# Kernel optimization log

Hardware: AMD Instinct MI355X
Metric: run time of the kernel (lower is better)

Reference implementation:

```python
import jax, jax.numpy as jnp
import numpy as np

IN_DIM = 256
HIDDEN = 512
MEM = 256
IN_LEN = 4096
THETA = 4096.0
BATCH = 32


def _expm(M):
    # scaling-and-squaring with Taylor series (float64)
    nrm = max(np.linalg.norm(M, 1), 1e-30)
    s = max(0, int(np.ceil(np.log2(nrm))) + 1)
    A = M / (2.0 ** s)
    d = M.shape[0]
    E = np.eye(d)
    term = np.eye(d)
    for k in range(1, 30):
        term = term @ A / k
        E = E + term
    for _ in range(s):
        E = E @ E
    return E


def _gen_AB(memory_size, theta):
    Q = np.arange(memory_size, dtype=np.float64).reshape(-1, 1)
    R = (2 * Q + 1) / theta
    i, j = np.meshgrid(Q, Q, indexing='ij')
    A = np.where(i < j, -1.0, (-1.0) ** (i - j + 1)) * R
    B = (-1.0) ** Q * R  # [mem, 1]
    # ZOH discretization with dt=1: expm of augmented [[A,B],[0,0]]
    d = memory_size
    em = np.zeros((d + 1, d + 1))
    em[:d, :d] = A
    em[:d, d:] = B
    ed = _expm(em)
    Ad = ed[:d, :d]
    Bd = ed[:d, d:]
    return Ad, Bd


def _impulse(memory_size, in_len, theta):
    Ad, Bd = _gen_AB(memory_size, theta)
    H = np.empty((memory_size, in_len), dtype=np.float64)
    v = Bd.copy()  # [mem, 1]
    for t in range(in_len):
        H[:, t] = v[:, 0]
        v = Ad @ v
    return H.astype(np.float32)


def setup_inputs() -> dict:
    key = jax.random.key(0)
    kx, ku, kh = jax.random.split(key, 3)
    x = jax.random.normal(kx, (BATCH, IN_LEN, IN_DIM), dtype=jnp.float32)
    W_u = jax.random.normal(ku, (1, IN_DIM), dtype=jnp.float32)
    W_h = jax.random.normal(kh, (HIDDEN, MEM + IN_DIM), dtype=jnp.float32)
    H = jnp.asarray(_impulse(MEM, IN_LEN, THETA))  # [mem, in_len]
    return {"x": x, "W_u": W_u, "W_h": W_h, "H": H}


def reference(x, W_u, W_h, H):
    batch, n, _ = x.shape
    # encode: u = relu(x @ W_u^T)  -> [B, n, 1]
    u = jax.nn.relu(jnp.einsum('bni,oi->bno', x, W_u))
    # FFT long convolution with impulse response H
    u_fft = jnp.fft.rfft(u.transpose(0, 2, 1), n=2 * n, axis=-1)  # [B,1,n+1]
    H_fft = jnp.fft.rfft(H, n=2 * n, axis=-1)                      # [mem,n+1]
    m = jnp.fft.irfft(u_fft * H_fft[None], n=2 * n, axis=-1)       # [B,mem,2n]
    m = m[:, :, :n].transpose(0, 2, 1)                             # [B,n,mem]
    # output head: h = relu([m, x] @ W_h^T)
    input_h = jnp.concatenate((m, x), axis=-1)                     # [B,n,mem+in_dim]
    h = jax.nn.relu(jnp.einsum('bnc,oc->bno', input_h, W_h))       # [B,n,hidden]
    h_n = h[:, -1, :]
    return (h, h_n)
```

## Files before the change

### kernel.cpp

```cpp
#include <hip/hip_runtime.h>
#include <hip/hip_bf16.h>
#include <math.h>


#define BATCH 32
#define T     4096
#define IND   256
#define HID   512
#define MEM   256
#define FFT_N 8192
#define FFT_LOG 13
#define BT    131072

typedef __attribute__((ext_vector_type(8))) short short8;
typedef __attribute__((ext_vector_type(8))) _Float16 half8;
typedef __attribute__((ext_vector_type(4))) float f32x4;

__device__ inline short f2bf(float f) {
    unsigned u = __float_as_uint(f);
    unsigned r = (u + 0x7FFFu + ((u >> 16) & 1u)) >> 16;
    return (short)r;
}
__device__ inline unsigned pk2h(float a, float b) {
    union { _Float16 h[2]; unsigned u; } v;
    v.h[0] = (_Float16)a; v.h[1] = (_Float16)b;
    return v.u;
}

__global__ __launch_bounds__(256) void relu_u_kernel(const float* __restrict__ x,
                                                     const float* __restrict__ Wu,
                                                     float* __restrict__ u,
                                                     _Float16* __restrict__ xh) {
    int wave = threadIdx.x >> 6, lane = threadIdx.x & 63;
    int r = blockIdx.x * 4 + wave;
    const float4 xv = *(const float4*)(x + (size_t)r * IND + lane * 4);
    const float4 wv = *(const float4*)(Wu + lane * 4);
    union { _Float16 h[4]; uint2 u2; } hv;
    hv.h[0] = (_Float16)xv.x; hv.h[1] = (_Float16)xv.y;
    hv.h[2] = (_Float16)xv.z; hv.h[3] = (_Float16)xv.w;
    *(uint2*)(xh + (size_t)r * IND + lane * 4) = hv.u2;
    float acc = xv.x * wv.x + xv.y * wv.y + xv.z * wv.z + xv.w * wv.w;
    for (int off = 32; off; off >>= 1) acc += __shfl_down(acc, off);
    if (lane == 0) u[r] = fmaxf(acc, 0.f);
}

__global__ __launch_bounds__(256) void wh_half_kernel(const float* __restrict__ Wh,
                                                      _Float16* __restrict__ whf) {
    int i = blockIdx.x * 256 + threadIdx.x;
    float4 v = *(const float4*)(Wh + (size_t)i * 4);
    union { _Float16 h[4]; uint2 u2; } hv;
    hv.h[0] = (_Float16)v.x; hv.h[1] = (_Float16)v.y;
    hv.h[2] = (_Float16)v.z; hv.h[3] = (_Float16)v.w;
    *(uint2*)(whf + (size_t)i * 4) = hv.u2;
}

__device__ void fft_fwd_r4(float* re, float* im) {
    __syncthreads();
    {
        const float fm = -(float)M_PI / 4096.f;
#pragma unroll
        for (int s = 0; s < 8; ++s) {
            int k = threadIdx.x + s * 512;
            float sn, cs; __sincosf(fm * (float)k, &sn, &cs);
            float ar = re[k], ai = im[k], br = re[k + 4096], bi = im[k + 4096];
            re[k] = ar + br; im[k] = ai + bi;
            float dr = ar - br, di = ai - bi;
            re[k + 4096] = cs * dr - sn * di;
            im[k + 4096] = cs * di + sn * dr;
        }
        __syncthreads();
    }
    for (int st = 10; st >= 0; st -= 2) {
        int q = 1 << st;
        float fm = -(float)M_PI / (float)(2 * q);
#pragma unroll
        for (int s = 0; s < 4; ++s) {
            int k = threadIdx.x + s * 512;
            int j = k & (q - 1);
            int i0 = ((k >> st) << (st + 2)) + j;
            float ar = re[i0],         ai = im[i0];
            float br = re[i0 + q],     bi = im[i0 + q];
            float cr = re[i0 + 2 * q], ci = im[i0 + 2 * q];
            float dr = re[i0 + 3 * q], di = im[i0 + 3 * q];
            float t0r = ar + cr, t0i = ai + ci;
            float t1r = ar - cr, t1i = ai - ci;
            float t2r = br + dr, t2i = bi + di;
            float t3r = bi - di, t3i = dr - br;
            float sn, cs; __sincosf(fm * (float)j, &sn, &cs);
            float w2r = cs * cs - sn * sn, w2i = 2.f * cs * sn;
            float w3r = w2r * cs - w2i * sn, w3i = w2r * sn + w2i * cs;
            re[i0] = t0r + t2r;               im[i0] = t0i + t2i;
            float er = t0r - t2r, ei = t0i - t2i;
            re[i0 + q] = er * w2r - ei * w2i; im[i0 + q] = er * w2i + ei * w2r;
            float fr = t1r + t3r, fi = t1i + t3i;
            re[i0 + 2 * q] = fr * cs - fi * sn; im[i0 + 2 * q] = fr * sn + fi * cs;
            float gr = t1r - t3r, gi = t1i - t3i;
            re[i0 + 3 * q] = gr * w3r - gi * w3i; im[i0 + 3 * q] = gr * w3i + gi * w3r;
        }
        __syncthreads();
    }
}
__device__ void fft_inv_r4(float* re, float* im) {
    __syncthreads();
    for (int st = 0; st <= 10; st += 2) {
        int q = 1 << st;
        float fm = (float)M_PI / (float)(2 * q);
#pragma unroll
        for (int s = 0; s < 4; ++s) {
            int k = threadIdx.x + s * 512;
            int j = k & (q - 1);
            int i0 = ((k >> st) << (st + 2)) + j;
            float Ar = re[i0],         Ai = im[i0];
            float Br = re[i0 + q],     Bi = im[i0 + q];
            float Cr = re[i0 + 2 * q], Ci = im[i0 + 2 * q];
            float Dr = re[i0 + 3 * q], Di = im[i0 + 3 * q];
            float sn, cs; __sincosf(fm * (float)j, &sn, &cs);
            float w2r = cs * cs - sn * sn, w2i = 2.f * cs * sn;
            float w3r = w2r * cs - w2i * sn, w3i = w2r * sn + w2i * cs;
            float bpr = Br * w2r - Bi * w2i, bpi = Br * w2i + Bi * w2r;
            float cpr = Cr * cs - Ci * sn,   cpi = Cr * sn + Ci * cs;
            float dpr = Dr * w3r - Di * w3i, dpi = Dr * w3i + Di * w3r;
            float t0r = Ar + bpr, t0i = Ai + bpi;
            float t2r = Ar - bpr, t2i = Ai - bpi;
            float t1r = cpr + dpr, t1i = cpi + dpi;
            float t3r = cpr - dpr, t3i = cpi - dpi;
            re[i0]         = t0r + t1r; im[i0]         = t0i + t1i;
            re[i0 + 2 * q] = t0r - t1r; im[i0 + 2 * q] = t0i - t1i;
            re[i0 + q]     = t2r - t3i; im[i0 + q]     = t2i + t3r;
            re[i0 + 3 * q] = t2r + t3i; im[i0 + 3 * q] = t2i - t3r;
        }
        __syncthreads();
    }
    {
        const float fm = (float)M_PI / 4096.f;
#pragma unroll
        for (int s = 0; s < 8; ++s) {
            int k = threadIdx.x + s * 512;
            float sn, cs; __sincosf(fm * (float)k, &sn, &cs);
            float br = re[k + 4096], bi = im[k + 4096];
            float tr = cs * br - sn * bi, ti = cs * bi + sn * br;
            float ar = re[k], ai = im[k];
            re[k] = ar + tr;        im[k] = ai + ti;
            re[k + 4096] = ar - tr; im[k + 4096] = ai - ti;
        }
        __syncthreads();
    }
}

__global__ __launch_bounds__(512) void fwd_all_kernel(const float* __restrict__ u,
                                                      const float* __restrict__ H,
                                                      float2* __restrict__ Uf,
                                                      float2* __restrict__ Hf) {
    __shared__ float re[FFT_N];
    __shared__ float im[FFT_N];
    int r = blockIdx.x;
    const float* src = (r < BATCH) ? (u + (size_t)r * T) : (H + (size_t)(r - BATCH) * T);
    float2* dst = (r < BATCH) ? (Uf + (size_t)r * FFT_N) : (Hf + (size_t)(r - BATCH) * FFT_N);
    for (int i = threadIdx.x; i < FFT_N; i += 512) {
        re[i] = (i < T) ? src[i] : 0.f;
        im[i] = 0.f;
    }
    fft_fwd_r4(re, im);
    for (int i = threadIdx.x; i < FFT_N; i += 512) dst[i] = make_float2(re[i], im[i]);
}

__global__ __launch_bounds__(512) void conv_m_kernel(const float2* __restrict__ Uf,
                                                     const float2* __restrict__ Hf,
                                                     _Float16* __restrict__ m2) {
    int qb = blockIdx.x;
    int b  = blockIdx.y;
    __shared__ float re[FFT_N];
    __shared__ float im[FFT_N];
    const float2* Ub = Uf + (size_t)b * FFT_N;
    const float inv = 1.0f / (float)FFT_N;
    unsigned p0[8], p1[8], p2[8], p3[8];

#define DO_FF(FF, PK)                                                          \
    {                                                                          \
        const float2* Ha = Hf + (size_t)(qb * 8 + 2 * (FF)) * FFT_N;           \
        const float2* Hb = Ha + FFT_N;                                         \
        for (int f = threadIdx.x; f < FFT_N; f += 512) {                       \
            float2 uv = Ub[f], h0 = Ha[f], h1 = Hb[f];                         \
            float gr = h0.x - h1.y, gi = h0.y + h1.x;           \
            re[f] = uv.x * gr - uv.y * gi;                                     \
            im[f] = uv.x * gi + uv.y * gr;                                     \
        }                                                                      \
        fft_inv_r4(re, im);                                                    \
        _Pragma("unroll")                                                      \
        for (int it = 0; it < 8; ++it) {                                       \
            int tt = threadIdx.x + it * 512;                                   \
            PK[it] = pk2h(re[tt] * inv, im[tt] * inv);                         \
        }                                                                      \
    }

    DO_FF(0, p0)
    DO_FF(1, p1)
    DO_FF(2, p2)
    DO_FF(3, p3)
#undef DO_FF

    _Float16* dst = m2 + ((size_t)qb * BT + (size_t)b * T) * 8;
#pragma unroll
    for (int it = 0; it < 8; ++it) {
        int tt = threadIdx.x + it * 512;
        uint4 w;
        w.x = p0[it]; w.y = p1[it]; w.z = p2[it]; w.w = p3[it];
        *(uint4*)(dst + (size_t)tt * 8) = w;
    }
}

__global__ __launch_bounds__(256) void h_gemm_kernel(const _Float16* __restrict__ xh,
                                                     const _Float16* __restrict__ whf,
                                                     const _Float16* __restrict__ m2,
                                                     float* __restrict__ out) {
    int bn = blockIdx.x;
    int bm = blockIdx.y;
    int t = threadIdx.x;
    int wv = t >> 6, lane = t & 63;
    int wm = (wv & 1) * 64, wn = (wv >> 1) * 64;
    int ln = lane & 15, kg = lane >> 4;
    int row0 = bm * 128 + wm + ln;
    int col0 = bn * 128 + wn + ln;

    f32x4 acc[4][4] = {};
#pragma unroll
    for (int kc = 0; kc < HID; kc += 32) {
        half8 af[4], bf[4];
        if (kc < MEM) {
#pragma unroll
            for (int i = 0; i < 4; ++i)
                af[i] = *(const half8*)(m2 + ((size_t)(kc / 8 + kg) * BT + row0 + i * 16) * 8);
        } else {
#pragma unroll
            for (int i = 0; i < 4; ++i)
                af[i] = *(const half8*)(xh + (size_t)(row0 + i * 16) * IND + (kc - MEM) + kg * 8);
        }
#pragma unroll
        for (int j = 0; j < 4; ++j)
            bf[j] = *(const half8*)(whf + (size_t)(col0 + j * 16) * HID + kc + kg * 8);
#pragma unroll
        for (int i = 0; i < 4; ++i)
#pragma unroll
            for (int j = 0; j < 4; ++j)
                acc[i][j] = __builtin_amdgcn_mfma_f32_16x16x32_f16(af[i], bf[j], acc[i][j], 0, 0, 0);
    }
#pragma unroll
    for (int i = 0; i < 4; ++i) {
#pragma unroll
        for (int j = 0; j < 4; ++j) {
#pragma unroll
            for (int r = 0; r < 4; ++r) {
                int row = bm * 128 + wm + i * 16 + kg * 4 + r;
                int col = bn * 128 + wn + j * 16 + ln;
                float v = fmaxf(acc[i][j][r], 0.f);
                out[(size_t)row * HID + col] = v;
                if ((row & (T - 1)) == (T - 1))
                    out[(size_t)BATCH * T * HID + (size_t)(row >> 12) * HID + col] = v;
            }
        }
    }
}

__device__ void fft_dif_fwd(float* re, float* im) {
    __syncthreads();
    for (int st = FFT_LOG; st >= 1; --st) {
        int half = 1 << (st - 1);
        float fm = -(float)M_PI / (float)half;
        for (int k = threadIdx.x; k < FFT_N / 2; k += 512) {
            int j  = k & (half - 1);
            int i1 = ((k >> (st - 1)) << st) + j;
            int i2 = i1 + half;
            float sn, cs;
            __sincosf(fm * (float)j, &sn, &cs);
            float ar = re[i1], ai = im[i1];
            float br = re[i2], bi = im[i2];
            re[i1] = ar + br; im[i1] = ai + bi;
            float dr = ar - br, di = ai - bi;
            re[i2] = cs * dr - sn * di;
            im[i2] = cs * di + sn * dr;
        }
        __syncthreads();
    }
}
__device__ void fft_dit_inv(float* re, float* im) {
    __syncthreads();
    for (int st = 1; st <= FFT_LOG; ++st) {
        int half = 1 << (st - 1);
        float fm = (float)M_PI / (float)half;
        for (int k = threadIdx.x; k < FFT_N / 2; k += 512) {
            int j  = k & (half - 1);
            int i1 = ((k >> (st - 1)) << st) + j;
            int i2 = i1 + half;
            float sn, cs;
            __sincosf(fm * (float)j, &sn, &cs);
            float br = re[i2], bi = im[i2];
            float tr = cs * br - sn * bi;
            float ti = cs * bi + sn * br;
            float ar = re[i1], ai = im[i1];
            re[i1] = ar + tr; im[i1] = ai + ti;
            re[i2] = ar - tr; im[i2] = ai - ti;
        }
        __syncthreads();
    }
}
__global__ __launch_bounds__(512) void fft_u_kernel(const float* __restrict__ u,
                                                    float2* __restrict__ Uf) {
    int b = blockIdx.x;
    __shared__ float re[FFT_N];
    __shared__ float im[FFT_N];
    for (int i = threadIdx.x; i < FFT_N; i += 512) {
        re[i] = i < T ? u[(size_t)b * T + i] : 0.f;
        im[i] = 0.f;
    }
    fft_dif_fwd(re, im);
    for (int i = threadIdx.x; i < FFT_N; i += 512)
        Uf[(size_t)b * FFT_N + i] = make_float2(re[i], im[i]);
}
__global__ __launch_bounds__(512) void g_fft_kernel(const float* __restrict__ Wh,
                                                    const float* __restrict__ H,
                                                    float2* __restrict__ Gf) {
    int o = blockIdx.x;
    __shared__ float re[FFT_N];
    __shared__ float im[FFT_N];
    const float* wrow = Wh + (size_t)o * HID;
    float acc[8];
#pragma unroll
    for (int d = 0; d < 8; ++d) acc[d] = 0.f;
    for (int q = 0; q < 256; ++q) {
        float w = wrow[q];
        const float* hrow = H + (size_t)q * T;
#pragma unroll
        for (int d = 0; d < 8; ++d)
            acc[d] = fmaf(w, hrow[threadIdx.x + d * 512], acc[d]);
    }
#pragma unroll
    for (int d = 0; d < 8; ++d) {
        re[threadIdx.x + d * 512] = acc[d];
        im[threadIdx.x + d * 512] = 0.f;
    }
    for (int i = T + threadIdx.x; i < FFT_N; i += 512) { re[i] = 0.f; im[i] = 0.f; }
    fft_dif_fwd(re, im);
    for (int i = threadIdx.x; i < FFT_N; i += 512)
        Gf[(size_t)o * FFT_N + i] = make_float2(re[i], im[i]);
}
__global__ __launch_bounds__(256) void xw_gemm_kernel(const float* __restrict__ x,
                                                      const float* __restrict__ Wh,
                                                      float* __restrict__ out) {
    __shared__ __align__(16) short Asl[4][128][8];
    __shared__ __align__(16) short Bsl[4][128][8];
    int bn = blockIdx.x;
    int bm = blockIdx.y;
    int t = threadIdx.x;
    int wv = t >> 6, lane = t & 63;
    int wm = (wv & 1) * 64, wn = (wv >> 1) * 64;
    int ln = lane & 15, kg = lane >> 4;
    f32x4 acc[4][4] = {};
    int mrow = t >> 1, khalf = t & 1;
    for (int kc = 0; kc < IND; kc += 32) {
        {
            const float* xr = x + ((size_t)(bm * 128 + mrow)) * IND + kc + khalf * 16;
            float4 v0 = *(const float4*)(xr + 0);
            float4 v1 = *(const float4*)(xr + 4);
            float4 v2 = *(const float4*)(xr + 8);
            float4 v3 = *(const float4*)(xr + 12);
            short8 s0 = { f2bf(v0.x), f2bf(v0.y), f2bf(v0.z), f2bf(v0.w),
                          f2bf(v1.x), f2bf(v1.y), f2bf(v1.z), f2bf(v1.w) };
            short8 s1 = { f2bf(v2.x), f2bf(v2.y), f2bf(v2.z), f2bf(v2.w),
                          f2bf(v3.x), f2bf(v3.y), f2bf(v3.z), f2bf(v3.w) };
            const float* wr = Wh + ((size_t)(bn * 128 + mrow)) * HID + 256 + kc + khalf * 16;
            float4 w0 = *(const float4*)(wr + 0);
            float4 w1 = *(const float4*)(wr + 4);
            float4 w2 = *(const float4*)(wr + 8);
            float4 w3 = *(const float4*)(wr + 12);
            short8 b0 = { f2bf(w0.x), f2bf(w0.y), f2bf(w0.z), f2bf(w0.w),
                          f2bf(w1.x), f2bf(w1.y), f2bf(w1.z), f2bf(w1.w) };
            short8 b1 = { f2bf(w2.x), f2bf(w2.y), f2bf(w2.z), f2bf(w2.w),
                          f2bf(w3.x), f2bf(w3.y), f2bf(w3.z), f2bf(w3.w) };
            __syncthreads();
            *(short8*)&Asl[khalf * 2 + 0][mrow][0] = s0;
            *(short8*)&Asl[khalf * 2 + 1][mrow][0] = s1;
            *(short8*)&Bsl[khalf * 2 + 0][mrow][0] = b0;
            *(short8*)&Bsl[khalf * 2 + 1][mrow][0] = b1;
            __syncthreads();
        }
        short8 af[4], bf[4];
#pragma unroll
        for (int i = 0; i < 4; ++i) af[i] = *(short8*)&Asl[kg][wm + i * 16 + ln][0];
#pragma unroll
        for (int j = 0; j < 4; ++j) bf[j] = *(short8*)&Bsl[kg][wn + j * 16 + ln][0];
#pragma unroll
        for (int i = 0; i < 4; ++i)
#pragma unroll
            for (int j = 0; j < 4; ++j)
                acc[i][j] = __builtin_amdgcn_mfma_f32_16x16x32_bf16(af[i], bf[j], acc[i][j], 0, 0, 0);
    }
#pragma unroll
    for (int i = 0; i < 4; ++i) {
#pragma unroll
        for (int j = 0; j < 4; ++j) {
#pragma unroll
            for (int r = 0; r < 4; ++r) {
                int row = bm * 128 + wm + i * 16 + (lane >> 4) * 4 + r;
                int col = bn * 128 + wn + j * 16 + (lane & 15);
                out[(size_t)row * HID + col] = acc[i][j][r];
            }
        }
    }
}
__global__ __launch_bounds__(512) void conv_apply_kernel(const float2* __restrict__ Uf,
                                                         const float2* __restrict__ Gf,
                                                         float* __restrict__ out) {
    int p = blockIdx.x;
    int b = blockIdx.y;
    __shared__ float re[FFT_N];
    __shared__ float im[FFT_N];
    const float2* Ub = Uf + (size_t)b * FFT_N;
    const float2* G0 = Gf + (size_t)(2 * p) * FFT_N;
    const float2* G1 = Gf + (size_t)(2 * p + 1) * FFT_N;
    for (int f = threadIdx.x; f < FFT_N; f += 512) {
        float2 uv = Ub[f], g0 = G0[f], g1 = G1[f];
        float gr = g0.x - g1.y, gi = g0.y + g1.x;
        re[f] = uv.x * gr - uv.y * gi;
        im[f] = uv.x * gi + uv.y * gr;
    }
    fft_dit_inv(re, im);
    const float inv = 1.0f / (float)FFT_N;
    for (int t = threadIdx.x; t < T; t += 512) {
        size_t idx = ((size_t)(b * T + t)) * HID + 2 * p;
        float2 xw = *(const float2*)(out + idx);
        float v0 = fmaxf(fmaf(re[t], inv, xw.x), 0.f);
        float v1 = fmaxf(fmaf(im[t], inv, xw.y), 0.f);
        *(float2*)(out + idx) = make_float2(v0, v1);
        if (t == T - 1) {
            size_t hn = (size_t)BATCH * T * HID + (size_t)b * HID + 2 * p;
            *(float2*)(out + hn) = make_float2(v0, v1);
        }
    }
}

extern "C" void kernel_launch(void* const* d_in, const int* in_sizes, int n_in,
                              void* d_out, int out_size, void* d_ws, size_t ws_size,
                              hipStream_t stream) {
    const float* x  = (const float*)d_in[0];
    const float* Wu = (const float*)d_in[1];
    const float* Wh = (const float*)d_in[2];
    const float* H  = (const float*)d_in[3];
    float* out = (float*)d_out;

    char* ws = (char*)d_ws;

    const size_t off_u   = 0;
    const size_t off_xh  = off_u  + 524288;
    const size_t off_whf = off_xh + 67108864;
    const size_t off_U   = off_whf + 524288;
    const size_t off_Hf  = off_U  + 2097152;
    const size_t off_m2  = off_Hf + 16777216;
    const size_t need    = off_m2 + (size_t)MEM * BT * 2;

    if (ws_size >= need) {
        float*     ws_u   = (float*)(ws + off_u);
        _Float16*  ws_xh  = (_Float16*)(ws + off_xh);
        _Float16*  ws_whf = (_Float16*)(ws + off_whf);
        float2*    ws_U   = (float2*)(ws + off_U);
        float2*    ws_Hf  = (float2*)(ws + off_Hf);
        _Float16*  ws_m2  = (_Float16*)(ws + off_m2);

        wh_half_kernel<<<HID * HID / 4 / 256, 256, 0, stream>>>(Wh, ws_whf);
        relu_u_kernel<<<BT / 4, 256, 0, stream>>>(x, Wu, ws_u, ws_xh);
        fwd_all_kernel<<<BATCH + MEM, 512, 0, stream>>>(ws_u, H, ws_U, ws_Hf);
        conv_m_kernel<<<dim3(MEM / 8, BATCH), 512, 0, stream>>>(ws_U, ws_Hf, ws_m2);
        h_gemm_kernel<<<dim3(HID / 128, BT / 128), 256, 0, stream>>>(ws_xh, ws_whf, ws_m2, out);
    } else {
        float*  ws_u = (float*)ws;
        float2* ws_U = (float2*)(ws + 524288);
        float2* ws_G = (float2*)(ws + 524288 + 2097152);
        relu_u_kernel<<<BT / 4, 256, 0, stream>>>(x, Wu, ws_u, (_Float16*)(ws + 524288 + 2097152 + 33554432));
        fft_u_kernel<<<BATCH, 512, 0, stream>>>(ws_u, ws_U);
        g_fft_kernel<<<HID, 512, 0, stream>>>(Wh, H, ws_G);
        xw_gemm_kernel<<<dim3(HID / 128, BATCH * T / 128), 256, 0, stream>>>(x, Wh, out);
        conv_apply_kernel<<<dim3(HID / 2, BATCH), 512, 0, stream>>>(ws_U, ws_G, out);
    }
}
```

Measured before the change: 740.6 us.

## Stage GEMM operand tiles in LDS via direct global-to-LDS loads

The output GEMM now cooperatively loads 128x64 A and B tiles into shared memory with global_load_lds, instead of each wave fetching its MFMA fragments straight from global memory. W_h is repacked into a k-group-major fp16 layout so the B tile loads are contiguous. Operands are now reused from LDS across the waves of a block, at the cost of two barriers per k-step and no double buffering. The fallback path gets a relu kernel that skips the unused fp16 copy of x.

```diff
diff --git a/kernel.cpp b/kernel.cpp
--- a/kernel.cpp
+++ b/kernel.cpp
@@ -25,6 +25,10 @@
     union { _Float16 h[2]; unsigned u; } v;
     v.h[0] = (_Float16)a; v.h[1] = (_Float16)b;
     return v.u;
+}
+__device__ __forceinline__ void gl_lds16(const void* g, void* l) {
+    __builtin_amdgcn_global_load_lds((const __attribute__((address_space(1))) unsigned*)g,
+                                     (__attribute__((address_space(3))) unsigned*)l, 16, 0, 0);
 }
 
 __global__ __launch_bounds__(256) void relu_u_kernel(const float* __restrict__ x,
@@ -43,15 +47,27 @@
     for (int off = 32; off; off >>= 1) acc += __shfl_down(acc, off);
     if (lane == 0) u[r] = fmaxf(acc, 0.f);
 }
-
-__global__ __launch_bounds__(256) void wh_half_kernel(const float* __restrict__ Wh,
-                                                      _Float16* __restrict__ whf) {
+__global__ __launch_bounds__(256) void relu_u_only_kernel(const float* __restrict__ x,
+                                                          const float* __restrict__ Wu,
+                                                          float* __restrict__ u) {
+    int wave = threadIdx.x >> 6, lane = threadIdx.x & 63;
+    int r = blockIdx.x * 4 + wave;
+    const float4 xv = *(const float4*)(x + (size_t)r * IND + lane * 4);
+    const float4 wv = *(const float4*)(Wu + lane * 4);
+    float acc = xv.x * wv.x + xv.y * wv.y + xv.z * wv.z + xv.w * wv.w;
+    for (int off = 32; off; off >>= 1) acc += __shfl_down(acc, off);
+    if (lane == 0) u[r] = fmaxf(acc, 0.f);
+}
+
+__global__ __launch_bounds__(256) void wh_pack_kernel(const float* __restrict__ Wh,
+                                                      _Float16* __restrict__ whfT) {
     int i = blockIdx.x * 256 + threadIdx.x;
-    float4 v = *(const float4*)(Wh + (size_t)i * 4);
-    union { _Float16 h[4]; uint2 u2; } hv;
-    hv.h[0] = (_Float16)v.x; hv.h[1] = (_Float16)v.y;
-    hv.h[2] = (_Float16)v.z; hv.h[3] = (_Float16)v.w;
-    *(uint2*)(whf + (size_t)i * 4) = hv.u2;
+    int col = i >> 7;
+    int kq  = (i & 127) << 2;
+    float4 v = *(const float4*)(Wh + (size_t)col * HID + kq);
+    _Float16* d = whfT + (size_t)(kq >> 3) * (HID * 8) + (size_t)col * 8 + (kq & 7);
+    d[0] = (_Float16)v.x; d[1] = (_Float16)v.y;
+    d[2] = (_Float16)v.z; d[3] = (_Float16)v.w;
 }
 
 __device__ void fft_fwd_r4(float* re, float* im) {
@@ -210,39 +226,61 @@
 }
 
 __global__ __launch_bounds__(256) void h_gemm_kernel(const _Float16* __restrict__ xh,
-                                                     const _Float16* __restrict__ whf,
+                                                     const _Float16* __restrict__ whfT,
                                                      const _Float16* __restrict__ m2,
                                                      float* __restrict__ out) {
+    __shared__ __align__(16) _Float16 As[8][128][8];
+    __shared__ __align__(16) _Float16 Bs[8][128][8];
     int bn = blockIdx.x;
     int bm = blockIdx.y;
     int t = threadIdx.x;
     int wv = t >> 6, lane = t & 63;
     int wm = (wv & 1) * 64, wn = (wv >> 1) * 64;
     int ln = lane & 15, kg = lane >> 4;
-    int row0 = bm * 128 + wm + ln;
-    int col0 = bn * 128 + wn + ln;
 
     f32x4 acc[4][4] = {};
 #pragma unroll
-    for (int kc = 0; kc < HID; kc += 32) {
-        half8 af[4], bf[4];
-        if (kc < MEM) {
+    for (int ks = 0; ks < 8; ++ks) {
+        int kc = ks * 64;
+        __syncthreads();
+#pragma unroll
+        for (int q = 0; q < 8; ++q) {
+            int c = wv * 8 + q;
+            int g = (c & 15) >> 1;
+            int rg = c & 1;
+            int row = rg * 64 + lane;
+            if (c < 16) {
+                const void* src;
+                if (kc < MEM)
+                    src = m2 + ((size_t)(kc / 8 + g) * BT + (size_t)bm * 128 + row) * 8;
+                else
+                    src = xh + (size_t)(bm * 128 + row) * IND + (kc - MEM) + g * 8;
+                gl_lds16(src, &As[g][rg * 64][0]);
+            } else {
+                const void* src = whfT + (size_t)(kc / 8 + g) * (HID * 8)
+                                       + (size_t)(bn * 128 + row) * 8;
+                gl_lds16(src, &Bs[g][rg * 64][0]);
+            }
+        }
+        __syncthreads();
+        half8 af[2][4], bf[2][4];
+#pragma unroll
+        for (int kk = 0; kk < 2; ++kk) {
 #pragma unroll
             for (int i = 0; i < 4; ++i)
-                af[i] = *(const half8*)(m2 + ((size_t)(kc / 8 + kg) * BT + row0 + i * 16) * 8);
-        } else {
+                af[kk][i] = *(const half8*)&As[kk * 4 + kg][wm + i * 16 + ln][0];
+#pragma unroll
+            for (int j = 0; j < 4; ++j)
+                bf[kk][j] = *(const half8*)&Bs[kk * 4 + kg][wn + j * 16 + ln][0];
+        }
+#pragma unroll
+        for (int kk = 0; kk < 2; ++kk)
 #pragma unroll
             for (int i = 0; i < 4; ++i)
-                af[i] = *(const half8*)(xh + (size_t)(row0 + i * 16) * IND + (kc - MEM) + kg * 8);
-        }
-#pragma unroll
-        for (int j = 0; j < 4; ++j)
-            bf[j] = *(const half8*)(whf + (size_t)(col0 + j * 16) * HID + kc + kg * 8);
-#pragma unroll
-        for (int i = 0; i < 4; ++i)
-#pragma unroll
-            for (int j = 0; j < 4; ++j)
-                acc[i][j] = __builtin_amdgcn_mfma_f32_16x16x32_f16(af[i], bf[j], acc[i][j], 0, 0, 0);
+#pragma unroll
+                for (int j = 0; j < 4; ++j)
+                    acc[i][j] = __builtin_amdgcn_mfma_f32_16x16x32_f16(af[kk][i], bf[kk][j],
+                                                                       acc[i][j], 0, 0, 0);
     }
 #pragma unroll
     for (int i = 0; i < 4; ++i) {
@@ -458,23 +496,23 @@
     const size_t need    = off_m2 + (size_t)MEM * BT * 2;
 
     if (ws_size >= need) {
-        float*     ws_u   = (float*)(ws + off_u);
-        _Float16*  ws_xh  = (_Float16*)(ws + off_xh);
-        _Float16*  ws_whf = (_Float16*)(ws + off_whf);
-        float2*    ws_U   = (float2*)(ws + off_U);
-        float2*    ws_Hf  = (float2*)(ws + off_Hf);
-        _Float16*  ws_m2  = (_Float16*)(ws + off_m2);
-
-        wh_half_kernel<<<HID * HID / 4 / 256, 256, 0, stream>>>(Wh, ws_whf);
+        float*     ws_u    = (float*)(ws + off_u);
+        _Float16*  ws_xh   = (_Float16*)(ws + off_xh);
+        _Float16*  ws_whfT = (_Float16*)(ws + off_whf);
+        float2*    ws_U    = (float2*)(ws + off_U);
+        float2*    ws_Hf   = (float2*)(ws + off_Hf);
+        _Float16*  ws_m2   = (_Float16*)(ws + off_m2);
+
+        wh_pack_kernel<<<HID * HID / 4 / 256, 256, 0, stream>>>(Wh, ws_whfT);
         relu_u_kernel<<<BT / 4, 256, 0, stream>>>(x, Wu, ws_u, ws_xh);
         fwd_all_kernel<<<BATCH + MEM, 512, 0, stream>>>(ws_u, H, ws_U, ws_Hf);
         conv_m_kernel<<<dim3(MEM / 8, BATCH), 512, 0, stream>>>(ws_U, ws_Hf, ws_m2);
-        h_gemm_kernel<<<dim3(HID / 128, BT / 128), 256, 0, stream>>>(ws_xh, ws_whf, ws_m2, out);
+        h_gemm_kernel<<<dim3(HID / 128, BT / 128), 256, 0, stream>>>(ws_xh, ws_whfT, ws_m2, out);
     } else {
         float*  ws_u = (float*)ws;
         float2* ws_U = (float2*)(ws + 524288);
         float2* ws_G = (float2*)(ws + 524288 + 2097152);
-        relu_u_kernel<<<BT / 4, 256, 0, stream>>>(x, Wu, ws_u, (_Float16*)(ws + 524288 + 2097152 + 33554432));
+        relu_u_only_kernel<<<BT / 4, 256, 0, stream>>>(x, Wu, ws_u);
         fft_u_kernel<<<BATCH, 512, 0, stream>>>(ws_u, ws_U);
         g_fft_kernel<<<HID, 512, 0, stream>>>(Wh, H, ws_G);
         xw_gemm_kernel<<<dim3(HID / 128, BATCH * T / 128), 256, 0, stream>>>(x, Wh, out);
```

Measured after the change: 668.8 us. 1.11x faster.
